# Kernel tuning notes

Hardware: AMD Instinct MI355X
Metric: run time of the kernel (lower is better)

The kernel has to match this reference:

```python
import jax, jax.numpy as jnp
import numpy as np

B, N, H = 8, 1024, 512
NUM_HEADS = 8
HEAD_DIM = H // NUM_HEADS
NUM_BUCKETS = 64


def setup_inputs() -> dict:
    key = jax.random.key(0)
    ks = jax.random.split(key, 8)
    x = jax.random.normal(ks[0], (B, N, H), dtype=jnp.float32)
    timestamp = jnp.sort(
        jax.random.randint(ks[1], (B, N), 0, 1700000000, dtype=jnp.int64), axis=-1
    )
    attn_mask = jnp.tril(jnp.ones((N, N), dtype=bool))[None].repeat(B, axis=0)
    f1_w = jax.random.normal(ks[2], (4 * H, H), dtype=jnp.float32) * 0.02
    f1_b = jnp.zeros((4 * H,), dtype=jnp.float32)
    f2_w = jax.random.normal(ks[3], (H, H), dtype=jnp.float32) * 0.02
    f2_b = jnp.zeros((H,), dtype=jnp.float32)
    ts_w = jax.random.normal(ks[4], (NUM_BUCKETS + 1,), dtype=jnp.float32) * 0.02
    pos_w = jax.random.normal(ks[5], (2 * N - 1,), dtype=jnp.float32) * 0.02
    return {"x": x, "timestamp": timestamp, "attn_mask": attn_mask,
            "f1_w": f1_w, "f1_b": f1_b, "f2_w": f2_w, "f2_b": f2_b,
            "ts_w": ts_w, "pos_w": pos_w}


def _rel_bias(ts, ts_w, pos_w):
    # ts: [B, N] float (already divided by 1e9). Returns [B, N, N].
    n = ts.shape[1]
    # positional part: classic skew trick -> [N, N]
    padded = jnp.concatenate([pos_w, jnp.zeros((n,), pos_w.dtype)])  # [3N-1]
    t = jnp.tile(padded, n)[:-n].reshape(n, 3 * n - 2)
    rel_pos = t[:, n - 1:2 * n - 1]  # [N, N]
    # bucketized time part
    ext = jnp.concatenate([ts, ts[:, n - 1:n]], axis=1)  # [B, N+1]
    diff = ext[:, 1:, None] - ext[:, None, :-1]          # [B, N, N]
    bucket = jnp.floor(
        jnp.log(jnp.clip(jnp.abs(diff), 1.0, None)) / 0.301
    ).astype(jnp.int32)
    bucket = jnp.clip(bucket, 0, NUM_BUCKETS)
    rel_ts = ts_w[bucket]  # [B, N, N]
    return rel_pos[None] + rel_ts


def reference(x, timestamp, attn_mask, f1_w, f1_b, f2_w, f2_b, ts_w, pos_w):
    b, n, h = x.shape
    nh, hd = NUM_HEADS, HEAD_DIM
    proj = jnp.einsum('bnh,oh->bno', x, f1_w) + f1_b  # [B, N, 4H]
    act = jax.nn.silu(proj)
    U, Qp, Kp, Vp = jnp.split(act, 4, axis=-1)
    Q = Qp.reshape(b, n, nh, hd)
    K = Kp.reshape(b, n, nh, hd)
    V = Vp.reshape(b, n, nh, hd)
    scale = hd ** -0.5
    scores = jnp.einsum('bqhd,bkhd->bhqk', Q, K) * scale  # [B, H, N, N]
    ts = timestamp.astype(jnp.float32) / 1e9
    bias = _rel_bias(ts, ts_w, pos_w)  # [B, N, N]
    scores = scores + bias[:, None]
    w = jax.nn.silu(scores)
    w = jnp.where(attn_mask[:, None], w, 0.0)
    attn_out = jnp.einsum('bhqk,bkhd->bqhd', w, V).reshape(b, n, h)
    gated = attn_out * U
    return jnp.einsum('bnh,oh->bno', gated, f2_w) + f2_b
```

## Files before the change

### kernel.cpp

```cpp
#include <hip/hip_runtime.h>


#define DI __device__ __forceinline__

constexpr int Nn = 1024;
constexpr int Hh = 512;
constexpr int NHEADS = 8;
constexpr int HD = 64;
constexpr int O1 = 2048;

typedef __attribute__((ext_vector_type(8))) short bf16x8;
typedef __attribute__((ext_vector_type(4))) float f32x4;

DI float bf2f(unsigned int b) { return __uint_as_float(b << 16); }

DI unsigned int cvt_pk_bf16(float lo, float hi) {
  unsigned int r;
  asm("v_cvt_pk_bf16_f32 %0, %1, %2" : "=v"(r) : "v"(lo), "v"(hi));
  return r;
}

DI void gl_lds16(const unsigned short* gsrc, unsigned short* ldst) {
  __builtin_amdgcn_global_load_lds(
      (const __attribute__((address_space(1))) unsigned int*)gsrc,
      (__attribute__((address_space(3))) unsigned int*)ldst, 16, 0, 0);
}

__global__ __launch_bounds__(256)
void cvt3(const float* __restrict__ s0, unsigned short* __restrict__ d0, int n0,
          const float* __restrict__ s1, unsigned short* __restrict__ d1, int n1,
          const float* __restrict__ s2, unsigned short* __restrict__ d2, int n2) {
  const int i = (blockIdx.x * 256 + threadIdx.x) * 4;
  const float* s; unsigned short* d; int off;
  if (i < n0) { s = s0; d = d0; off = i; }
  else if (i < n0 + n1) { s = s1; d = d1; off = i - n0; }
  else if (i < n0 + n1 + n2) { s = s2; d = d2; off = i - n0 - n1; }
  else return;
  const float4 v = *(const float4*)(s + off);
  uint2 st;
  st.x = cvt_pk_bf16(v.x, v.y);
  st.y = cvt_pk_bf16(v.z, v.w);
  *(uint2*)(d + off) = st;
}

template<int BM, int BN, bool SILU, typename OutT>
__global__ __launch_bounds__(256)
void mfma_gemm_bt(const unsigned short* __restrict__ A,
                  const unsigned short* __restrict__ Bw,
                  OutT* __restrict__ C,
                  int M, int Nout, int K) {
  constexpr int MI = BM / 32, NJ = BN / 32;
  __shared__ unsigned short As[2][BM * 32];
  __shared__ unsigned short Bs[2][BN * 32];
  const int tid = threadIdx.x;
  const int wv = tid >> 6, lane = tid & 63;
  const int quad = lane >> 4, ln = lane & 15;
  const int wm = wv & 1, wn = wv >> 1;
  const int linb = blockIdx.x + gridDim.x * blockIdx.y;
  const int nwg = gridDim.x * gridDim.y;
  const int sw = (linb & 7) * (nwg >> 3) + (linb >> 3);
  const int m0 = (sw / gridDim.x) * BM, n0 = (sw % gridDim.x) * BN;
  const unsigned short* Asrc = A + (size_t)(m0 + wv * (BM / 4) + (lane >> 2)) * K + (lane & 3) * 8;
  const unsigned short* Bsrc = Bw + (size_t)(n0 + wv * (BN / 4) + (lane >> 2)) * K + (lane & 3) * 8;
  const int T = K / 32;

  f32x4 acc[MI][NJ] = {};
#pragma unroll
  for (int s = 0; s < BM / 64; ++s)
    gl_lds16(Asrc + (size_t)(s * 16) * K, &As[0][(wv * (BM / 4) + s * 16) * 32]);
#pragma unroll
  for (int s = 0; s < BN / 64; ++s)
    gl_lds16(Bsrc + (size_t)(s * 16) * K, &Bs[0][(wv * (BN / 4) + s * 16) * 32]);

  for (int t = 0; t < T; ++t) {
    const int p = t & 1;
    __syncthreads();
    if (t + 1 < T) {
      const int k1 = (t + 1) * 32;
#pragma unroll
      for (int s = 0; s < BM / 64; ++s)
        gl_lds16(Asrc + (size_t)(s * 16) * K + k1, &As[1 - p][(wv * (BM / 4) + s * 16) * 32]);
#pragma unroll
      for (int s = 0; s < BN / 64; ++s)
        gl_lds16(Bsrc + (size_t)(s * 16) * K + k1, &Bs[1 - p][(wv * (BN / 4) + s * 16) * 32]);
    }
    bf16x8 af[MI], bfr[NJ];
#pragma unroll
    for (int i = 0; i < MI; ++i)
      af[i] = *(const bf16x8*)&As[p][(wm * (BM / 2) + i * 16 + ln) * 32 + quad * 8];
#pragma unroll
    for (int j = 0; j < NJ; ++j)
      bfr[j] = *(const bf16x8*)&Bs[p][(wn * (BN / 2) + j * 16 + ln) * 32 + quad * 8];
#pragma unroll
    for (int i = 0; i < MI; ++i)
#pragma unroll
      for (int j = 0; j < NJ; ++j)
        acc[i][j] = __builtin_amdgcn_mfma_f32_16x16x32_bf16(af[i], bfr[j], acc[i][j], 0, 0, 0);
  }
#pragma unroll
  for (int i = 0; i < MI; ++i) {
#pragma unroll
    for (int r = 0; r < 4; ++r) {
      const size_t row = m0 + wm * (BM / 2) + i * 16 + quad * 4 + r;
#pragma unroll
      for (int j = 0; j < NJ; ++j) {
        float s = acc[i][j][r];
        if (SILU) s = s * __builtin_amdgcn_rcpf(1.f + __expf(-s));
        const int col = n0 + wn * (BN / 2) + j * 16 + ln;
        if (sizeof(OutT) == 2)
          ((unsigned short*)C)[row * Nout + col] = (unsigned short)cvt_pk_bf16(s, s);
        else
          ((float*)C)[row * Nout + col] = s;
      }
    }
  }
}

__global__ __launch_bounds__(512)
void attn_mfma(const unsigned short* __restrict__ act,
               const int* __restrict__ tsi,
               const float* __restrict__ ts_w,
               const float* __restrict__ pos_w,
               unsigned short* __restrict__ gated) {
  constexpr int LDT = 72;
  __shared__ __align__(16) unsigned short Ks[64 * LDT];
  __shared__ __align__(16) unsigned short Vt[64 * LDT];
  __shared__ __align__(16) unsigned short Ps[8][16 * LDT];
  __shared__ float posS[1088];
  __shared__ __align__(16) float tks[64];
  const int tid = threadIdx.x;
  const int wave = tid >> 6, lane = tid & 63;
  const int quad = lane >> 4, ln = lane & 15;
  const int grp = wave >> 2;
  const int wv4 = wave & 3;
  const int xb = blockIdx.x;
  const int ntiles = 16 - xb;
  const int qbase = (grp ? (15 - xb) : xb) * 64;
  const int h = blockIdx.y, b = blockIdx.z;
  const unsigned short* actb = act + (size_t)b * Nn * O1;
  const int mul = (tsi[1] == 0 && tsi[3] == 0 && tsi[5] == 0 && tsi[7] == 0) ? 2 : 1;
  for (int i = tid; i < 1088; i += 512) posS[i] = (i < 1024) ? pos_w[i] : 0.f;
  const float t0w = ts_w[0], t1w = ts_w[1];
  const float Cthr = 1.3512093f;
  const int qglob = qbase + wv4 * 16 + ln;
  float tq;
  {
    const int idx = (qglob + 1 < Nn) ? qglob + 1 : Nn - 1;
    tq = (float)tsi[(b * Nn + idx) * mul] / 1e9f;
  }
  const float Tthr = tq - Cthr;
  const unsigned short* qb = actb + (size_t)qglob * O1 + Hh + h * HD + quad * 8;
  const bf16x8 qf0 = *(const bf16x8*)qb, qf1 = *(const bf16x8*)(qb + 32);
  f32x4 zero = {0.f, 0.f, 0.f, 0.f};
  f32x4 o[4] = {zero, zero, zero, zero};

  const int kr = tid >> 3, dc = (tid & 7) * 8;
  const int vp = tid >> 4, vd4 = (tid & 15) * 4;

  uint4 ka; uint2 v0, v1; int tsv = 0;
  auto issue_loads = [&](int t) {
    const int k0 = t * 64;
    ka = *(const uint4*)(actb + (size_t)(k0 + kr) * O1 + 2 * Hh + h * HD + dc);
    const unsigned short* vg = actb + (size_t)(k0 + 2 * vp) * O1 + 3 * Hh + h * HD + vd4;
    v0 = *(const uint2*)vg;
    v1 = *(const uint2*)(vg + O1);
    if (tid < 64) tsv = tsi[(b * Nn + k0 + tid) * mul];
  };
  auto stage = [&]() {
    *(uint4*)&Ks[kr * LDT + dc] = ka;
    const unsigned int lo[2] = {v0.x, v0.y}, hi[2] = {v1.x, v1.y};
#pragma unroll
    for (int u = 0; u < 4; ++u) {
      const int d = vd4 + u;
      const int rot = ((vp >> 2) + (d >> 3)) & 7;
      const unsigned int sel = (u & 1) ? 0x07060302u : 0x05040100u;
      *(unsigned int*)&Vt[d * LDT + 2 * (rot * 4 + (vp & 3))] =
          __builtin_amdgcn_perm(hi[u >> 1], lo[u >> 1], sel);
    }
    if (tid < 64) tks[tid] = (float)tsv / 1e9f;
  };
  auto tile_compute = [&](int k0, bool mtile) {
#pragma unroll
    for (int n0i = 0; n0i < 4; ++n0i) {
      const int n0 = n0i * 16;
      const bf16x8 kf0 = *(const bf16x8*)&Ks[(n0 + ln) * LDT + quad * 8];
      const bf16x8 kf1 = *(const bf16x8*)&Ks[(n0 + ln) * LDT + 32 + quad * 8];
      f32x4 s = {0.f, 0.f, 0.f, 0.f};
      __builtin_amdgcn_s_setprio(1);
      s = __builtin_amdgcn_mfma_f32_16x16x32_bf16(kf0, qf0, s, 0, 0, 0);
      s = __builtin_amdgcn_mfma_f32_16x16x32_bf16(kf1, qf1, s, 0, 0, 0);
      __builtin_amdgcn_s_setprio(0);
      const f32x4 tk4 = *(const f32x4*)&tks[n0 + quad * 4];
      const int pb = 1023 + k0 + n0 + quad * 4 - qglob;
      float w[4];
#pragma unroll
      for (int r = 0; r < 4; ++r) {
        const float tsb = (tk4[r] <= Tthr) ? t1w : t0w;
        const float sv = s[r] * 0.125f + (posS[pb + r] + tsb);
        float ww = sv * __builtin_amdgcn_rcpf(1.f + __expf(-sv));
        if (mtile) {
          const bool valid = (k0 + n0 + quad * 4 + r <= qglob);
          ww = valid ? ww : 0.f;
        }
        w[r] = ww;
      }
      uint2 pk;
      pk.x = cvt_pk_bf16(w[0], w[1]);
      pk.y = cvt_pk_bf16(w[2], w[3]);
      *(uint2*)&Ps[wave][ln * LDT + n0 + quad * 4] = pk;
    }
#pragma unroll
    for (int kkh = 0; kkh < 2; ++kkh) {
      const int kk0 = kkh * 32;
      const bf16x8 pa = *(const bf16x8*)&Ps[wave][ln * LDT + kk0 + quad * 8];
      __builtin_amdgcn_s_setprio(1);
#pragma unroll
      for (int j = 0; j < 4; ++j) {
        const int d = j * 16 + ln;
        const bf16x8 vbf = *(const bf16x8*)
            &Vt[d * LDT + 8 * ((quad + (kk0 >> 3) + (d >> 3)) & 7)];
        o[j] = __builtin_amdgcn_mfma_f32_16x16x32_bf16(pa, vbf, o[j], 0, 0, 0);
      }
      __builtin_amdgcn_s_setprio(0);
    }
  };

  issue_loads(0);
  for (int t = 0; t < ntiles; ++t) {
    stage();
    if (t + 1 < ntiles) issue_loads(t + 1);
    __syncthreads();
    if (grp || t <= xb)
      tile_compute(t * 64, grp ? (t == ntiles - 1) : (t == xb));
    if (t + 1 < ntiles) __syncthreads();
  }
#pragma unroll
  for (int dsub = 0; dsub < 4; ++dsub) {
#pragma unroll
    for (int r = 0; r < 4; ++r) {
      const int q = qbase + wv4 * 16 + quad * 4 + r;
      const int d = dsub * 16 + ln;
      const float u = bf2f((unsigned int)actb[(size_t)q * O1 + h * HD + d]);
      gated[((size_t)b * Nn + q) * Hh + h * HD + d] =
          (unsigned short)cvt_pk_bf16(o[dsub][r] * u, o[dsub][r] * u);
    }
  }
}

extern "C" void kernel_launch(void* const* d_in, const int* in_sizes, int n_in,
                              void* d_out, int out_size, void* d_ws, size_t ws_size,
                              hipStream_t stream) {
  const float* x    = (const float*)d_in[0];
  const int*   tsi  = (const int*)d_in[1];
  const float* f1w  = (const float*)d_in[3];
  const float* f2w  = (const float*)d_in[5];
  const float* tsw  = (const float*)d_in[7];
  const float* posw = (const float*)d_in[8];
  char* ws = (char*)d_ws;
  unsigned short* act   = (unsigned short*)ws;
  unsigned short* xb    = (unsigned short*)(ws + ((size_t)32 << 20));
  unsigned short* gated = xb;
  unsigned short* f1wb  = (unsigned short*)(ws + ((size_t)40 << 20));
  unsigned short* f2wb  = (unsigned short*)(ws + ((size_t)42 << 20));
  float* out = (float*)d_out;

  constexpr int NX = 8192 * 512, NW1 = 2048 * 512, NW2 = 512 * 512;
  cvt3<<<(NX + NW1 + NW2) / 4 / 256, 256, 0, stream>>>(
      x, xb, NX, f1w, f1wb, NW1, f2w, f2wb, NW2);
  mfma_gemm_bt<128, 128, true, unsigned short>
      <<<dim3(O1 / 128, 8192 / 128), 256, 0, stream>>>(xb, f1wb, act, 8192, O1, Hh);
  attn_mfma<<<dim3(8, NHEADS, 8), 512, 0, stream>>>(
      act, tsi, tsw, posw, gated);
  mfma_gemm_bt<64, 64, false, float>
      <<<dim3(Hh / 64, 8192 / 64), 256, 0, stream>>>(gated, f2wb, out, 8192, Hh, Hh);
}
```

Baseline: 177.8 us.

## Replace first projection GEMM with 256x256 double-buffered phased MFMA kernel

Adds a dedicated kernel for the x·f1_wᵀ + SiLU projection that uses 256x256 tiles, 8 waves, and double-buffered LDS. Global-to-LDS loads for the next K tile are interleaved across four compute phases, with fine-grained vmcnt waits and s_setprio around the MFMA bursts. The block index is also swizzled for L2 locality. The aim is to overlap memory traffic with MFMA work and raise data reuse per tile. The cost is heavy LDS use (128KB) and register pressure, which limit occupancy, plus only 256 blocks in the grid.

```diff
diff --git a/kernel.cpp b/kernel.cpp
--- a/kernel.cpp
+++ b/kernel.cpp
@@ -111,6 +111,118 @@
           ((unsigned short*)C)[row * Nout + col] = (unsigned short)cvt_pk_bf16(s, s);
         else
           ((float*)C)[row * Nout + col] = s;
+      }
+    }
+  }
+}
+
+template<int I0>
+DI void g1_rdA(bf16x8 (&af)[4][2], const unsigned short* Asp,
+               int wm, int ln, int quad) {
+#pragma unroll
+  for (int i = 0; i < 4; ++i)
+#pragma unroll
+    for (int h = 0; h < 2; ++h)
+      af[i][h] = *(const bf16x8*)
+          &Asp[(wm * 128 + (I0 + i) * 16 + ln) * 64 + h * 32 + quad * 8];
+}
+template<int J0>
+DI void g1_rdB(bf16x8 (&bf)[2][2], const unsigned short* Bsp,
+               int wn, int ln, int quad) {
+#pragma unroll
+  for (int j = 0; j < 2; ++j)
+#pragma unroll
+    for (int h = 0; h < 2; ++h)
+      bf[j][h] = *(const bf16x8*)
+          &Bsp[(wn * 64 + (J0 + j) * 16 + ln) * 64 + h * 32 + quad * 8];
+}
+template<int I0, int J0>
+DI void g1_mm(f32x4 (&acc)[8][4], bf16x8 (&af)[4][2], bf16x8 (&bf)[2][2]) {
+  __builtin_amdgcn_s_setprio(1);
+#pragma unroll
+  for (int h = 0; h < 2; ++h)
+#pragma unroll
+    for (int i = 0; i < 4; ++i)
+#pragma unroll
+      for (int j = 0; j < 2; ++j)
+        acc[I0 + i][J0 + j] = __builtin_amdgcn_mfma_f32_16x16x32_bf16(
+            af[i][h], bf[j][h], acc[I0 + i][J0 + j], 0, 0, 0);
+  __builtin_amdgcn_s_setprio(0);
+}
+
+__global__ __launch_bounds__(512)
+void gemm1_8ph(const unsigned short* __restrict__ A,
+               const unsigned short* __restrict__ Bw,
+               unsigned short* __restrict__ C) {
+  constexpr int Nout = O1, K = Hh, BM = 256, BN = 256, BK = 64;
+  __shared__ __align__(16) unsigned short As[2][BM * BK];
+  __shared__ __align__(16) unsigned short Bs[2][BN * BK];
+  const int tid = threadIdx.x;
+  const int lane = tid & 63, wv = tid >> 6;
+  const int quad = lane >> 4, ln = lane & 15;
+  const int wm = wv >> 2, wn = wv & 3;
+  const int linb = blockIdx.x + gridDim.x * blockIdx.y;
+  const int nwg = gridDim.x * gridDim.y;
+  const int sw = (linb & 7) * (nwg >> 3) + (linb >> 3);
+  const int m0 = (sw / gridDim.x) * BM, n0 = (sw % gridDim.x) * BN;
+  const int srow = tid >> 3, scol = (tid & 7) * 8;
+  const unsigned short* Ab = A + (size_t)(m0 + srow) * K + scol;
+  const unsigned short* Bb = Bw + (size_t)(n0 + srow) * K + scol;
+  constexpr int nt = K / BK;
+
+  auto issA = [&](int t, int r, int p) {
+    gl_lds16(Ab + (size_t)(r * 64) * K + t * BK,
+             &As[p][(r * 64 + srow) * BK + scol]);
+  };
+  auto issB = [&](int t, int r, int p) {
+    gl_lds16(Bb + (size_t)(r * 64) * K + t * BK,
+             &Bs[p][(r * 64 + srow) * BK + scol]);
+  };
+
+  f32x4 acc[8][4] = {};
+  bf16x8 af[4][2], bf[2][2];
+
+  issB(0, 0, 0); issB(0, 1, 0); issB(0, 2, 0); issB(0, 3, 0);
+  issA(0, 0, 0); issA(0, 2, 0); issA(0, 1, 0); issA(0, 3, 0);
+  asm volatile("s_waitcnt vmcnt(0)" ::: "memory");
+  asm volatile("s_barrier" ::: "memory");
+
+  for (int t = 0; t < nt; ++t) {
+    const int p = t & 1;
+    const bool pf = (t + 1 < nt);
+    asm volatile("s_waitcnt vmcnt(2)" ::: "memory");
+    asm volatile("s_barrier" ::: "memory");
+    g1_rdA<0>(af, As[p], wm, ln, quad);
+    g1_rdB<0>(bf, Bs[p], wn, ln, quad);
+    g1_mm<0, 0>(acc, af, bf);
+    if (pf) { issB(t + 1, 0, 1 - p); issB(t + 1, 1, 1 - p); }
+    asm volatile("s_barrier" ::: "memory");
+    g1_rdB<2>(bf, Bs[p], wn, ln, quad);
+    g1_mm<0, 2>(acc, af, bf);
+    if (pf) { issB(t + 1, 2, 1 - p); issB(t + 1, 3, 1 - p); }
+    if (pf) asm volatile("s_waitcnt vmcnt(4)" ::: "memory");
+    else    asm volatile("s_waitcnt vmcnt(0)" ::: "memory");
+    asm volatile("s_barrier" ::: "memory");
+    g1_rdA<4>(af, As[p], wm, ln, quad);
+    g1_rdB<0>(bf, Bs[p], wn, ln, quad);
+    g1_mm<4, 0>(acc, af, bf);
+    if (pf) { issA(t + 1, 0, 1 - p); issA(t + 1, 2, 1 - p); }
+    asm volatile("s_barrier" ::: "memory");
+    g1_rdB<2>(bf, Bs[p], wn, ln, quad);
+    g1_mm<4, 2>(acc, af, bf);
+    if (pf) { issA(t + 1, 1, 1 - p); issA(t + 1, 3, 1 - p); }
+  }
+#pragma unroll
+  for (int i = 0; i < 8; ++i) {
+#pragma unroll
+    for (int r = 0; r < 4; ++r) {
+      const size_t row = (size_t)m0 + wm * 128 + i * 16 + quad * 4 + r;
+#pragma unroll
+      for (int j = 0; j < 4; ++j) {
+        float s = acc[i][j][r];
+        s = s * __builtin_amdgcn_rcpf(1.f + __expf(-s));
+        C[row * Nout + n0 + wn * 64 + j * 16 + ln] =
+            (unsigned short)cvt_pk_bf16(s, s);
       }
     }
   }
@@ -267,8 +379,7 @@
   constexpr int NX = 8192 * 512, NW1 = 2048 * 512, NW2 = 512 * 512;
   cvt3<<<(NX + NW1 + NW2) / 4 / 256, 256, 0, stream>>>(
       x, xb, NX, f1w, f1wb, NW1, f2w, f2wb, NW2);
-  mfma_gemm_bt<128, 128, true, unsigned short>
-      <<<dim3(O1 / 128, 8192 / 128), 256, 0, stream>>>(xb, f1wb, act, 8192, O1, Hh);
+  gemm1_8ph<<<dim3(O1 / 256, 8192 / 256), 512, 0, stream>>>(xb, f1wb, act);
   attn_mfma<<<dim3(8, NHEADS, 8), 512, 0, stream>>>(
       act, tsi, tsw, posw, gated);
   mfma_gemm_bt<64, 64, false, float>
```

Measured after the change: 178.5 us. About the same (+0.4%).
